# Kernel optimization log

Hardware: AMD Instinct MI355X
Metric: run time of the kernel (lower is better)

Reference implementation:

```python
import jax, jax.numpy as jnp
import numpy as np

N_NODES = 50000
N_GRAPHS = 512

def _glorot(key, shape):
    fan_in, fan_out = shape[1], shape[0]
    lim = np.sqrt(6.0 / (fan_in + fan_out))
    return jax.random.uniform(key, shape, jnp.float32, -lim, lim)

def setup_inputs() -> dict:
    key = jax.random.key(0)
    ks = jax.random.split(key, 12)
    x = jax.random.normal(ks[0], (N_NODES, 128), jnp.float32)
    edge_index = jax.random.randint(ks[1], (2, 800000), 0, N_NODES, jnp.int64)
    batch = jnp.sort(jax.random.randint(ks[2], (N_NODES,), 0, N_GRAPHS, jnp.int64))
    return {
        "x": x,
        "edge_index": edge_index,
        "batch": batch,
        "W1": _glorot(ks[3], (256, 128)), "b1": jnp.zeros((256,), jnp.float32),
        "W2": _glorot(ks[4], (256, 256)), "b2": jnp.zeros((256,), jnp.float32),
        "W3": _glorot(ks[5], (256, 256)), "b3": jnp.zeros((256,), jnp.float32),
        "Wf1": _glorot(ks[6], (128, 256)), "bf1": jnp.zeros((128,), jnp.float32),
        "Wf2": _glorot(ks[7], (10, 128)), "bf2": jnp.zeros((10,), jnp.float32),
    }

def _gin_conv(h, edge_index, W, b):
    # GINConv (eps=0): lin(x_i + sum_{j in N(i)} x_j)
    src, dst = edge_index[0], edge_index[1]
    aggr = jax.ops.segment_sum(h[src], dst, num_segments=N_NODES)
    return (h + aggr) @ W.T + b

def reference(x, edge_index, batch, W1, b1, W2, b2, W3, b3, Wf1, bf1, Wf2, bf2):
    h = jax.nn.relu(_gin_conv(x, edge_index, W1, b1))
    h = jax.nn.relu(_gin_conv(h, edge_index, W2, b2))
    h = jax.nn.relu(_gin_conv(h, edge_index, W3, b3))
    # global mean pool over graphs
    sums = jax.ops.segment_sum(h, batch, num_segments=N_GRAPHS)
    counts = jax.ops.segment_sum(jnp.ones((N_NODES,), h.dtype), batch, num_segments=N_GRAPHS)
    hg = sums / jnp.maximum(counts, 1.0)[:, None]
    h = jax.nn.relu(hg @ Wf1.T + bf1)
    return h @ Wf2.T + bf2
```

## Files before the change

kernel.cpp:

```cpp
#include <hip/hip_runtime.h>

#define N_NODES 50000
#define N_GRAPHS 512
#define N_EDGES 800000
#define NBKT 49
#define BKT_CAP 20480

typedef __attribute__((ext_vector_type(8))) short short8;
typedef __attribute__((ext_vector_type(8))) unsigned short ushort8;
typedef __attribute__((ext_vector_type(4))) float floatx4;
typedef __attribute__((ext_vector_type(2))) float floatx2;

__device__ __forceinline__ float bf2f(unsigned short u) {
    union { unsigned int i; float f; } c;
    c.i = ((unsigned int)u) << 16;
    return c.f;
}
__device__ __forceinline__ unsigned short f2bf(float f) {
    union { float f; unsigned int i; } c;
    c.f = f;
    unsigned int u = c.i;
    return (unsigned short)((u + 0x7fffu + ((u >> 16) & 1u)) >> 16);
}

__device__ __forceinline__ unsigned char ftofp8(float f) {
    union { float f; unsigned int u; } c; c.f = f;
    unsigned int s = (c.u >> 24) & 0x80u;
    float a = fabsf(f);
    if (a < 0x1p-6f) return (unsigned char)s;
    if (a > 448.f)   return (unsigned char)(s | 0x7E);
    unsigned int u = c.u & 0x7FFFFFFFu;
    unsigned int r = u + 0x7FFFFu + ((u >> 20) & 1u);
    return (unsigned char)(s | (((r >> 23) - 120u) << 3) | ((r >> 20) & 7u));
}

__device__ __forceinline__ void f8acc(float* acc, uint2 v) {
    floatx2 a = __builtin_amdgcn_cvt_pk_f32_fp8(v.x, false);
    floatx2 b = __builtin_amdgcn_cvt_pk_f32_fp8(v.x, true);
    floatx2 c = __builtin_amdgcn_cvt_pk_f32_fp8(v.y, false);
    floatx2 d = __builtin_amdgcn_cvt_pk_f32_fp8(v.y, true);
    acc[0] += a[0]; acc[1] += a[1]; acc[2] += b[0]; acc[3] += b[1];
    acc[4] += c[0]; acc[5] += c[1]; acc[6] += d[0]; acc[7] += d[1];
}

__device__ __forceinline__ void g2lds16(const unsigned short* g, void* lds) {
    __builtin_amdgcn_global_load_lds(
        (const __attribute__((address_space(1))) void*)g,
        (__attribute__((address_space(3))) void*)lds, 16, 0, 0);
}

__global__ void conv_all(const float* __restrict__ x, const float* __restrict__ W1,
                         const float* __restrict__ W2, const float* __restrict__ W3,
                         unsigned char* __restrict__ xf8, unsigned short* __restrict__ o1,
                         unsigned short* __restrict__ o2, unsigned short* __restrict__ o3,
                         float4* __restrict__ sums4, int* __restrict__ bktcnt) {
    int i = blockIdx.x * blockDim.x + threadIdx.x;
    if (i >= 1640960) {
        int j = i - 1640960;
        if (j < 32768) sums4[j] = make_float4(0.f, 0.f, 0.f, 0.f);
        else if (j < 32832) bktcnt[j - 32768] = 0;
        return;
    }
    if (i < 1600000) {
        float4 v = ((const float4*)x)[i];
        uchar4 o;
        o.x = ftofp8(v.x); o.y = ftofp8(v.y); o.z = ftofp8(v.z); o.w = ftofp8(v.w);
        ((uchar4*)xf8)[i] = o;
        return;
    }
    int j = i - 1600000;
    const float* src; unsigned short* out; int base;
    if (j < 8192)       { src = W1; out = o1; base = j; }
    else if (j < 24576) { src = W2; out = o2; base = j - 8192; }
    else                { src = W3; out = o3; base = j - 24576; }
    float4 v = ((const float4*)src)[base];
    ushort4 o;
    o.x = f2bf(v.x); o.y = f2bf(v.y); o.z = f2bf(v.z); o.w = f2bf(v.w);
    ((ushort4*)out)[base] = o;
}

__global__ __launch_bounds__(256) void bin_edges(const int* __restrict__ src,
                                                 const int* __restrict__ dst,
                                                 int* __restrict__ bktcnt,
                                                 unsigned int* __restrict__ staging) {
    __shared__ int cnt[NBKT];
    __shared__ int base[NBKT];
    int t = threadIdx.x;
    if (t < NBKT) cnt[t] = 0;
    __syncthreads();
    int e0 = blockIdx.x * 2048;
    int d[8], s[8];
#pragma unroll
    for (int r = 0; r < 8; r++) {
        int e = e0 + r * 256 + t;
        if (e < N_EDGES) {
            d[r] = dst[e]; s[r] = src[e];
            atomicAdd(&cnt[d[r] >> 10], 1);
        } else d[r] = -1;
    }
    __syncthreads();
    if (t < NBKT) base[t] = cnt[t] ? atomicAdd(&bktcnt[t], cnt[t]) : 0;
    __syncthreads();
#pragma unroll
    for (int r = 0; r < 8; r++) {
        if (d[r] >= 0) {
            int bkt = d[r] >> 10;
            int off = atomicAdd(&base[bkt], 1);
            staging[(size_t)bkt * BKT_CAP + off] = ((unsigned)d[r] << 16) | (unsigned)s[r];
        }
    }
}

__global__ __launch_bounds__(1024) void bucket_build(
    const unsigned int* __restrict__ staging, const int* __restrict__ bktcnt,
    int* __restrict__ rowptr, unsigned short* __restrict__ csr) {
    __shared__ int hist[1024];
    __shared__ int s[1024];
    __shared__ int bse[64];
    __shared__ int lcur[1024];
    int b = blockIdx.x, t = threadIdx.x;
    if (t < 64) {
        int orig = (t < NBKT) ? bktcnt[t] : 0;
        int v = orig;
        for (int off = 1; off < 64; off <<= 1) {
            int u = __shfl_up(v, off, 64);
            if (t >= off) v += u;
        }
        bse[t] = v - orig;
    }
    hist[t] = 0;
    __syncthreads();
    int base = bse[b];
    int cnt = bktcnt[b];
    int n0 = b << 10;
    const unsigned int* stg = staging + (size_t)b * BKT_CAP;
    for (int p = t; p < cnt; p += 1024)
        atomicAdd(&hist[(stg[p] >> 16) - n0], 1);
    __syncthreads();
    int v = hist[t];
    s[t] = v;
    __syncthreads();
    for (int off = 1; off < 1024; off <<= 1) {
        int add = (t >= off) ? s[t - off] : 0;
        __syncthreads();
        s[t] += add;
        __syncthreads();
    }
    int excl = s[t] - v;
    int node = n0 + t;
    if (node < N_NODES) rowptr[node] = base + excl;
    lcur[t] = base + excl;
    if (b == NBKT - 1 && t == 0) rowptr[N_NODES] = N_EDGES;
    __syncthreads();
    for (int p = t; p < cnt; p += 1024) {
        unsigned e = stg[p];
        int li = (int)(e >> 16) - n0;
        int pos = atomicAdd(&lcur[li], 1);
        csr[pos] = (unsigned short)(e & 0xFFFFu);
    }
}

template <int C>
__global__ __launch_bounds__(256) void gather_f8(const unsigned char* __restrict__ h,
                                                 const int* __restrict__ rowptr,
                                                 const unsigned short* __restrict__ csr,
                                                 unsigned short* __restrict__ agg) {
    const int TPN = C / 8;
    const int NPB = 256 / TPN;
    int t = threadIdx.x;
    int n = blockIdx.x * NPB + t / TPN;
    if (n >= N_NODES) return;
    int c8 = t % TPN;
    const uint2* hp = (const uint2*)h + c8;
    float acc[8];
#pragma unroll
    for (int j = 0; j < 8; j++) acc[j] = 0.f;
    f8acc(acc, hp[(size_t)n * TPN]);
    int p = rowptr[n], end = rowptr[n + 1];
    for (; p + 8 <= end; p += 8) {
        int j0 = csr[p],     j1 = csr[p + 1], j2 = csr[p + 2], j3 = csr[p + 3];
        int j4 = csr[p + 4], j5 = csr[p + 5], j6 = csr[p + 6], j7 = csr[p + 7];
        uint2 v0 = hp[(size_t)j0 * TPN];
        uint2 v1 = hp[(size_t)j1 * TPN];
        uint2 v2 = hp[(size_t)j2 * TPN];
        uint2 v3 = hp[(size_t)j3 * TPN];
        uint2 v4 = hp[(size_t)j4 * TPN];
        uint2 v5 = hp[(size_t)j5 * TPN];
        uint2 v6 = hp[(size_t)j6 * TPN];
        uint2 v7 = hp[(size_t)j7 * TPN];
        f8acc(acc, v0); f8acc(acc, v1); f8acc(acc, v2); f8acc(acc, v3);
        f8acc(acc, v4); f8acc(acc, v5); f8acc(acc, v6); f8acc(acc, v7);
    }
    for (; p + 4 <= end; p += 4) {
        int j0 = csr[p], j1 = csr[p + 1], j2 = csr[p + 2], j3 = csr[p + 3];
        uint2 v0 = hp[(size_t)j0 * TPN];
        uint2 v1 = hp[(size_t)j1 * TPN];
        uint2 v2 = hp[(size_t)j2 * TPN];
        uint2 v3 = hp[(size_t)j3 * TPN];
        f8acc(acc, v0); f8acc(acc, v1); f8acc(acc, v2); f8acc(acc, v3);
    }
    for (; p < end; ++p) {
        uint2 v = hp[(size_t)csr[p] * TPN];
        f8acc(acc, v);
    }
    ushort8 o;
#pragma unroll
    for (int j = 0; j < 8; j++) o[j] = f2bf(acc[j]);
    ((ushort8*)agg)[(size_t)n * TPN + c8] = o;
}

template <int K, int F8OUT>
__global__ __launch_bounds__(256) void gemm_mfma64(
    const unsigned short* __restrict__ A, const unsigned short* __restrict__ W,
    const float* __restrict__ bias, void* __restrict__ Cout, int M) {
    __shared__ short8 As[256];
    __shared__ short8 Ws[512];

    int tid = threadIdx.x;
    int wave = tid >> 6, lane = tid & 63;
    int wm = wave & 1, wn = wave >> 1;
    int rowbase = blockIdx.x * 64;
    int colbase = blockIdx.y * 128;
    int lkc = lane >> 4, lr = lane & 15;
    int rsw = lr ^ (lkc << 2);
    int rslot = lkc * 16 + rsw;

    int ar = rowbase + wave * 16 + rsw; if (ar >= M) ar = M - 1;
    int wr0 = colbase + (0 * 4 + wave) * 16 + rsw;
    int wr1 = colbase + (1 * 4 + wave) * 16 + rsw;
    char* asb  = (char*)As + (size_t)(wave * 64) * 16;
    char* wsb0 = (char*)Ws + (size_t)(0 * 256 + wave * 64) * 16;
    char* wsb1 = (char*)Ws + (size_t)(1 * 256 + wave * 64) * 16;

    floatx4 acc[2][4];
#pragma unroll
    for (int i = 0; i < 2; i++)
#pragma unroll
        for (int j = 0; j < 4; j++) acc[i][j] = (floatx4)(0.f);

#pragma unroll 2
    for (int k0 = 0; k0 < K; k0 += 32) {
        int ks = k0 + lkc * 8;
        g2lds16(A + (size_t)ar * K + ks, asb);
        g2lds16(W + (size_t)wr0 * K + ks, wsb0);
        g2lds16(W + (size_t)wr1 * K + ks, wsb1);
        __syncthreads();

        short8 af[2], wf[4];
#pragma unroll
        for (int mt = 0; mt < 2; mt++) af[mt] = As[(wm * 2 + mt) * 64 + rslot];
#pragma unroll
        for (int nt = 0; nt < 4; nt++) wf[nt] = Ws[(wn * 4 + nt) * 64 + rslot];
#pragma unroll
        for (int mt = 0; mt < 2; mt++)
#pragma unroll
            for (int nt = 0; nt < 4; nt++)
                acc[mt][nt] = __builtin_amdgcn_mfma_f32_16x16x32_bf16(
                    af[mt], wf[nt], acc[mt][nt], 0, 0, 0);
        __syncthreads();
    }

#pragma unroll
    for (int mt = 0; mt < 2; mt++) {
#pragma unroll
        for (int reg = 0; reg < 4; reg++) {
            int row = rowbase + (wm * 2 + mt) * 16 + lkc * 4 + reg;
            if (row >= M) continue;
#pragma unroll
            for (int nt = 0; nt < 4; nt++) {
                int col = colbase + (wn * 4 + nt) * 16 + lr;
                float v = fmaxf(acc[mt][nt][reg] + bias[col], 0.f);
                if (F8OUT)
                    ((unsigned char*)Cout)[(size_t)row * 256 + col] = ftofp8(v);
                else
                    ((unsigned short*)Cout)[(size_t)row * 256 + col] = f2bf(v);
            }
        }
    }
}

__global__ __launch_bounds__(256) void pool_accum(const unsigned short* __restrict__ h,
                                                  const int* __restrict__ batch,
                                                  float* __restrict__ sums) {
    int t = threadIdx.x;
    int r0 = blockIdx.x * 32;
    int r1 = r0 + 32; if (r1 > N_NODES) r1 = N_NODES;
    if (r0 >= N_NODES) return;
    float acc = 0.f;
    int gcur = batch[r0];
    for (int r = r0; r < r1; ++r) {
        int g = batch[r];
        if (g != gcur) { atomicAdd(&sums[gcur * 256 + t], acc); acc = 0.f; gcur = g; }
        acc += bf2f(h[(size_t)r * 256 + t]);
    }
    atomicAdd(&sums[gcur * 256 + t], acc);
}

__global__ __launch_bounds__(128) void head(const float* __restrict__ sums,
                                            const int* __restrict__ batch,
                                            const float* __restrict__ Wf1,
                                            const float* __restrict__ bf1,
                                            const float* __restrict__ Wf2,
                                            const float* __restrict__ bf2,
                                            float* __restrict__ out) {
    __shared__ float hg[256];
    __shared__ float hid[128];
    int g = blockIdx.x;
    int t = threadIdx.x;
    int lo = 0, hi = N_NODES;
    while (lo < hi) { int m = (lo + hi) >> 1; if (batch[m] < g) lo = m + 1; else hi = m; }
    int start = lo;
    lo = 0; hi = N_NODES;
    while (lo < hi) { int m = (lo + hi) >> 1; if (batch[m] < g + 1) lo = m + 1; else hi = m; }
    int end = lo;
    float inv = 1.0f / fmaxf((float)(end - start), 1.0f);
    hg[t]       = sums[g * 256 + t] * inv;
    hg[t + 128] = sums[g * 256 + t + 128] * inv;
    __syncthreads();
    float a1 = bf1[t];
    for (int c = 0; c < 256; c++) a1 += hg[c] * Wf1[t * 256 + c];
    hid[t] = fmaxf(a1, 0.f);
    __syncthreads();
    if (t < 10) {
        float a = bf2[t];
        for (int j = 0; j < 128; j++) a += hid[j] * Wf2[t * 128 + j];
        out[g * 10 + t] = a;
    }
}

extern "C" void kernel_launch(void* const* d_in, const int* in_sizes, int n_in,
                              void* d_out, int out_size, void* d_ws, size_t ws_size,
                              hipStream_t stream) {
    const float* x   = (const float*)d_in[0];
    const int*  edge = (const int*)d_in[1];
    const int*  batch= (const int*)d_in[2];
    const float* W1  = (const float*)d_in[3];
    const float* b1  = (const float*)d_in[4];
    const float* W2  = (const float*)d_in[5];
    const float* b2  = (const float*)d_in[6];
    const float* W3  = (const float*)d_in[7];
    const float* b3  = (const float*)d_in[8];
    const float* Wf1 = (const float*)d_in[9];
    const float* bf1 = (const float*)d_in[10];
    const float* Wf2 = (const float*)d_in[11];
    const float* bf2 = (const float*)d_in[12];
    const int* src = edge;
    const int* dst = edge + N_EDGES;

    char* wsb = (char*)d_ws;
    size_t off = 0;
    auto alloc = [&](size_t bytes) { void* p = wsb + off; off += (bytes + 255) & ~(size_t)255; return p; };
    unsigned char*  x_f8   = (unsigned char*)alloc((size_t)N_NODES * 128);
    unsigned char*  h1_f8  = (unsigned char*)alloc((size_t)N_NODES * 256);
    unsigned char*  h2_f8  = (unsigned char*)alloc((size_t)N_NODES * 256);
    unsigned short* agg_bf = (unsigned short*)alloc((size_t)N_NODES * 256 * 2);
    unsigned short* hA_bf  = (unsigned short*)alloc((size_t)N_NODES * 256 * 2);
    unsigned short* W1bf   = (unsigned short*)alloc(256 * 128 * 2);
    unsigned short* W2bf   = (unsigned short*)alloc(256 * 256 * 2);
    unsigned short* W3bf   = (unsigned short*)alloc(256 * 256 * 2);
    int* rowptr    = (int*)alloc((N_NODES + 4) * 4);
    unsigned short* csr = (unsigned short*)alloc((size_t)N_EDGES * 2);
    unsigned int* staging = (unsigned int*)alloc((size_t)NBKT * BKT_CAP * 4);
    int* bktcnt    = (int*)alloc(64 * 4);
    float* sums    = (float*)alloc((size_t)N_GRAPHS * 256 * 4);

    conv_all<<<(1673792 + 255) / 256, 256, 0, stream>>>(
        x, W1, W2, W3, x_f8, W1bf, W2bf, W3bf, (float4*)sums, bktcnt);

    bin_edges<<<(N_EDGES + 2047) / 2048, 256, 0, stream>>>(src, dst, bktcnt, staging);
    bucket_build<<<NBKT, 1024, 0, stream>>>(staging, bktcnt, rowptr, csr);

    dim3 ggrid((N_NODES + 63) / 64, 2);

    gather_f8<128><<<(N_NODES + 15) / 16, 256, 0, stream>>>(x_f8, rowptr, csr, agg_bf);
    gemm_mfma64<128, 1><<<ggrid, 256, 0, stream>>>(agg_bf, W1bf, b1, h1_f8, N_NODES);

    gather_f8<256><<<(N_NODES + 7) / 8, 256, 0, stream>>>(h1_f8, rowptr, csr, agg_bf);
    gemm_mfma64<256, 1><<<ggrid, 256, 0, stream>>>(agg_bf, W2bf, b2, h2_f8, N_NODES);

    gather_f8<256><<<(N_NODES + 7) / 8, 256, 0, stream>>>(h2_f8, rowptr, csr, agg_bf);
    gemm_mfma64<256, 0><<<ggrid, 256, 0, stream>>>(agg_bf, W3bf, b3, hA_bf, N_NODES);

    pool_accum<<<(N_NODES + 31) / 32, 256, 0, stream>>>(hA_bf, batch, sums);
    head<<<N_GRAPHS, 128, 0, stream>>>(sums, batch, Wf1, bf1, Wf2, bf2, (float*)d_out);
}
```

Before: 319.7 us.

## Fuse edge binning into conversion kernel and double GEMM K-step per barrier

The edge-binning work now runs in the same launch as the fp8/bf16 conversion kernel, with the extra blocks handling binning. Zeroing the bucket counters moves to a hipMemsetAsync issued before that launch. The MFMA GEMM now loads 64 K-columns per iteration into doubled LDS buffers, halving the number of barriers per tile. The aim is to cut launch overhead and synchronisation, in exchange for more LDS per block and an extra memset call.

```diff
diff --git a/kernel.cpp b/kernel.cpp
--- a/kernel.cpp
+++ b/kernel.cpp
@@ -49,16 +49,48 @@
         (__attribute__((address_space(3))) void*)lds, 16, 0, 0);
 }
 
-__global__ void conv_all(const float* __restrict__ x, const float* __restrict__ W1,
-                         const float* __restrict__ W2, const float* __restrict__ W3,
-                         unsigned char* __restrict__ xf8, unsigned short* __restrict__ o1,
-                         unsigned short* __restrict__ o2, unsigned short* __restrict__ o3,
-                         float4* __restrict__ sums4, int* __restrict__ bktcnt) {
-    int i = blockIdx.x * blockDim.x + threadIdx.x;
+#define NB_BIN 391
+__global__ __launch_bounds__(256) void prep_fused(
+    const float* __restrict__ x, const float* __restrict__ W1,
+    const float* __restrict__ W2, const float* __restrict__ W3,
+    const int* __restrict__ src, const int* __restrict__ dst,
+    unsigned char* __restrict__ xf8, unsigned short* __restrict__ o1,
+    unsigned short* __restrict__ o2, unsigned short* __restrict__ o3,
+    float4* __restrict__ sums4, int* __restrict__ bktcnt,
+    unsigned int* __restrict__ staging) {
+    int t = threadIdx.x;
+    if (blockIdx.x < NB_BIN) {
+        __shared__ int cnt[NBKT];
+        __shared__ int base[NBKT];
+        if (t < NBKT) cnt[t] = 0;
+        __syncthreads();
+        int e0 = blockIdx.x * 2048;
+        int d[8], s[8];
+#pragma unroll
+        for (int r = 0; r < 8; r++) {
+            int e = e0 + r * 256 + t;
+            if (e < N_EDGES) {
+                d[r] = dst[e]; s[r] = src[e];
+                atomicAdd(&cnt[d[r] >> 10], 1);
+            } else d[r] = -1;
+        }
+        __syncthreads();
+        if (t < NBKT) base[t] = cnt[t] ? atomicAdd(&bktcnt[t], cnt[t]) : 0;
+        __syncthreads();
+#pragma unroll
+        for (int r = 0; r < 8; r++) {
+            if (d[r] >= 0) {
+                int bkt = d[r] >> 10;
+                int off = atomicAdd(&base[bkt], 1);
+                staging[(size_t)bkt * BKT_CAP + off] = ((unsigned)d[r] << 16) | (unsigned)s[r];
+            }
+        }
+        return;
+    }
+    int i = (blockIdx.x - NB_BIN) * 256 + t;
     if (i >= 1640960) {
         int j = i - 1640960;
         if (j < 32768) sums4[j] = make_float4(0.f, 0.f, 0.f, 0.f);
-        else if (j < 32832) bktcnt[j - 32768] = 0;
         return;
     }
     if (i < 1600000) {
@@ -69,46 +101,14 @@
         return;
     }
     int j = i - 1600000;
-    const float* src; unsigned short* out; int base;
-    if (j < 8192)       { src = W1; out = o1; base = j; }
-    else if (j < 24576) { src = W2; out = o2; base = j - 8192; }
-    else                { src = W3; out = o3; base = j - 24576; }
-    float4 v = ((const float4*)src)[base];
+    const float* srcp; unsigned short* out; int base;
+    if (j < 8192)       { srcp = W1; out = o1; base = j; }
+    else if (j < 24576) { srcp = W2; out = o2; base = j - 8192; }
+    else                { srcp = W3; out = o3; base = j - 24576; }
+    float4 v = ((const float4*)srcp)[base];
     ushort4 o;
     o.x = f2bf(v.x); o.y = f2bf(v.y); o.z = f2bf(v.z); o.w = f2bf(v.w);
     ((ushort4*)out)[base] = o;
-}
-
-__global__ __launch_bounds__(256) void bin_edges(const int* __restrict__ src,
-                                                 const int* __restrict__ dst,
-                                                 int* __restrict__ bktcnt,
-                                                 unsigned int* __restrict__ staging) {
-    __shared__ int cnt[NBKT];
-    __shared__ int base[NBKT];
-    int t = threadIdx.x;
-    if (t < NBKT) cnt[t] = 0;
-    __syncthreads();
-    int e0 = blockIdx.x * 2048;
-    int d[8], s[8];
-#pragma unroll
-    for (int r = 0; r < 8; r++) {
-        int e = e0 + r * 256 + t;
-        if (e < N_EDGES) {
-            d[r] = dst[e]; s[r] = src[e];
-            atomicAdd(&cnt[d[r] >> 10], 1);
-        } else d[r] = -1;
-    }
-    __syncthreads();
-    if (t < NBKT) base[t] = cnt[t] ? atomicAdd(&bktcnt[t], cnt[t]) : 0;
-    __syncthreads();
-#pragma unroll
-    for (int r = 0; r < 8; r++) {
-        if (d[r] >= 0) {
-            int bkt = d[r] >> 10;
-            int off = atomicAdd(&base[bkt], 1);
-            staging[(size_t)bkt * BKT_CAP + off] = ((unsigned)d[r] << 16) | (unsigned)s[r];
-        }
-    }
 }
 
 __global__ __launch_bounds__(1024) void bucket_build(
@@ -213,8 +213,8 @@
 __global__ __launch_bounds__(256) void gemm_mfma64(
     const unsigned short* __restrict__ A, const unsigned short* __restrict__ W,
     const float* __restrict__ bias, void* __restrict__ Cout, int M) {
-    __shared__ short8 As[256];
-    __shared__ short8 Ws[512];
+    __shared__ short8 As[512];
+    __shared__ short8 Ws[1024];
 
     int tid = threadIdx.x;
     int wave = tid >> 6, lane = tid & 63;
@@ -228,9 +228,12 @@
     int ar = rowbase + wave * 16 + rsw; if (ar >= M) ar = M - 1;
     int wr0 = colbase + (0 * 4 + wave) * 16 + rsw;
     int wr1 = colbase + (1 * 4 + wave) * 16 + rsw;
-    char* asb  = (char*)As + (size_t)(wave * 64) * 16;
-    char* wsb0 = (char*)Ws + (size_t)(0 * 256 + wave * 64) * 16;
-    char* wsb1 = (char*)Ws + (size_t)(1 * 256 + wave * 64) * 16;
+    char* asb0 = (char*)As + (size_t)(0 * 256 + wave * 64) * 16;
+    char* asb1 = (char*)As + (size_t)(1 * 256 + wave * 64) * 16;
+    char* wsb00 = (char*)Ws + (size_t)(0 * 512 + 0 * 256 + wave * 64) * 16;
+    char* wsb01 = (char*)Ws + (size_t)(0 * 512 + 1 * 256 + wave * 64) * 16;
+    char* wsb10 = (char*)Ws + (size_t)(1 * 512 + 0 * 256 + wave * 64) * 16;
+    char* wsb11 = (char*)Ws + (size_t)(1 * 512 + 1 * 256 + wave * 64) * 16;
 
     floatx4 acc[2][4];
 #pragma unroll
@@ -239,24 +242,33 @@
         for (int j = 0; j < 4; j++) acc[i][j] = (floatx4)(0.f);
 
 #pragma unroll 2
-    for (int k0 = 0; k0 < K; k0 += 32) {
-        int ks = k0 + lkc * 8;
-        g2lds16(A + (size_t)ar * K + ks, asb);
-        g2lds16(W + (size_t)wr0 * K + ks, wsb0);
-        g2lds16(W + (size_t)wr1 * K + ks, wsb1);
-        __syncthreads();
-
-        short8 af[2], wf[4];
-#pragma unroll
-        for (int mt = 0; mt < 2; mt++) af[mt] = As[(wm * 2 + mt) * 64 + rslot];
-#pragma unroll
-        for (int nt = 0; nt < 4; nt++) wf[nt] = Ws[(wn * 4 + nt) * 64 + rslot];
-#pragma unroll
-        for (int mt = 0; mt < 2; mt++)
+    for (int k0 = 0; k0 < K; k0 += 64) {
+        int ks0 = k0 + lkc * 8;
+        int ks1 = k0 + 32 + lkc * 8;
+        g2lds16(A + (size_t)ar * K + ks0, asb0);
+        g2lds16(W + (size_t)wr0 * K + ks0, wsb00);
+        g2lds16(W + (size_t)wr1 * K + ks0, wsb01);
+        g2lds16(A + (size_t)ar * K + ks1, asb1);
+        g2lds16(W + (size_t)wr0 * K + ks1, wsb10);
+        g2lds16(W + (size_t)wr1 * K + ks1, wsb11);
+        __syncthreads();
+
+#pragma unroll
+        for (int h = 0; h < 2; h++) {
+            short8 af[2], wf[4];
+#pragma unroll
+            for (int mt = 0; mt < 2; mt++)
+                af[mt] = As[h * 256 + (wm * 2 + mt) * 64 + rslot];
 #pragma unroll
             for (int nt = 0; nt < 4; nt++)
-                acc[mt][nt] = __builtin_amdgcn_mfma_f32_16x16x32_bf16(
-                    af[mt], wf[nt], acc[mt][nt], 0, 0, 0);
+                wf[nt] = Ws[h * 512 + (wn * 4 + nt) * 64 + rslot];
+#pragma unroll
+            for (int mt = 0; mt < 2; mt++)
+#pragma unroll
+                for (int nt = 0; nt < 4; nt++)
+                    acc[mt][nt] = __builtin_amdgcn_mfma_f32_16x16x32_bf16(
+                        af[mt], wf[nt], acc[mt][nt], 0, 0, 0);
+        }
         __syncthreads();
     }
 
@@ -364,10 +376,12 @@
     int* bktcnt    = (int*)alloc(64 * 4);
     float* sums    = (float*)alloc((size_t)N_GRAPHS * 256 * 4);
 
-    conv_all<<<(1673792 + 255) / 256, 256, 0, stream>>>(
-        x, W1, W2, W3, x_f8, W1bf, W2bf, W3bf, (float4*)sums, bktcnt);
-
-    bin_edges<<<(N_EDGES + 2047) / 2048, 256, 0, stream>>>(src, dst, bktcnt, staging);
+    hipMemsetAsync(bktcnt, 0, 64 * sizeof(int), stream);
+    const int NB_CONV = 1673728 / 256;
+    prep_fused<<<NB_BIN + NB_CONV, 256, 0, stream>>>(
+        x, W1, W2, W3, src, dst, x_f8, W1bf, W2bf, W3bf,
+        (float4*)sums, bktcnt, staging);
+
     bucket_build<<<NBKT, 1024, 0, stream>>>(staging, bktcnt, rowptr, csr);
 
     dim3 ggrid((N_NODES + 63) / 64, 2);
```

Result: no change. 315.6 us, median of 2 (-1.3%).
